# Optimization experiments

Hardware: AMD Instinct MI355X
Metric: run time of the kernel (lower is better)

## Reference

```python
import jax, jax.numpy as jnp
import numpy as np

B, C, T = 8, 256, 8192
CALC, H = 256, 4
D = CALC // H  # head dim = 64
EPS = 1e-5


def setup_inputs() -> dict:
    key = jax.random.key(0)
    ks = jax.random.split(key, 5)
    return {
        "x": jax.random.normal(ks[0], (B, C, T), dtype=jnp.float32),
        "W_prenet": jax.random.normal(ks[1], (3 * CALC, C), dtype=jnp.float32) * 0.05,
        "W_proj": jax.random.normal(ks[2], (C, CALC), dtype=jnp.float32) * 0.05,
        "b_proj": jax.random.normal(ks[3], (C,), dtype=jnp.float32) * 0.05,
        "scale": jax.random.normal(ks[4], (1,), dtype=jnp.float32),
        "gamma": jnp.ones((C,), dtype=jnp.float32),
        "beta": jnp.zeros((C,), dtype=jnp.float32),
    }


def reference(x, W_prenet, W_proj, b_proj, scale, gamma, beta):
    residual = x
    # 1x1 conv prenet: [B, 3*CALC, T]
    h = jnp.einsum('oc,bct->bot', W_prenet, x)
    # split heads: channels grouped as H blocks of 3*D, then chunk into q/k/v of D each
    h = h.reshape(B, H, 3 * D, T)
    q = h[:, :, :D, :]            # [B,H,D,T]
    k = h[:, :, D:2 * D, :]
    v = h[:, :, 2 * D:, :]
    # softmax over time on keys (with the module's +1e-5 shift)
    k = jax.nn.softmax(k + EPS, axis=3)
    # keys @ values^T : [B,H,Dk,Dv]
    kv = jnp.einsum('bhdt,bhet->bhde', k, v)
    # kv^T @ queries  : [B,H,Dv,T]
    ctx = jnp.einsum('bhde,bhdt->bhet', kv, q)
    ctx = ctx.reshape(B, CALC, T)
    # 1x1 conv projection + bias
    out = jnp.einsum('oc,bct->bot', W_proj, ctx) + b_proj[None, :, None]
    out = scale * out  # learnable scalar gate
    # dropout is identity in eval mode
    out = out + residual
    # LayerNorm over channel axis with per-channel affine
    mean = jnp.mean(out, axis=1, keepdims=True)
    var = jnp.var(out, axis=1, keepdims=True)
    out = (out - mean) * jax.lax.rsqrt(var + EPS)
    out = out * gamma[None, :, None] + beta[None, :, None]
    return out
```

## Files before the change

kernel.cpp:

```cpp
#include <hip/hip_runtime.h>
#include <hip/hip_bf16.h>
#include <math.h>

#define BB 8
#define CC 256
#define TT 8192
#define EPSF 1e-5f

typedef short v8s __attribute__((ext_vector_type(8)));
typedef float v4f __attribute__((ext_vector_type(4)));

#define MFMA(a, b, c) __builtin_amdgcn_mfma_f32_16x16x32_bf16((a), (b), (c), 0, 0, 0)


#define OFF_WKV 0
#define OFF_WPJ 65536
#define OFF_UPART 98304
#define OFF_ZPART 4292608
#define OFF_KV 4358144
#define OFF_PT 4489216
#define OFF_MBF 4751360

__device__ __forceinline__ unsigned short f2bf(float f) {
  __hip_bfloat16 h = __float2bfloat16(f);
  return __builtin_bit_cast(unsigned short, h);
}
__device__ __forceinline__ float bf2f(unsigned short u) {
  return __bfloat162float(__builtin_bit_cast(__hip_bfloat16, u));
}

__global__ void k0_pack(const float* __restrict__ Wpre,
                        const float* __restrict__ Wproj,
                        float* __restrict__ ws) {
  const int r = blockIdx.x;
  const int c = threadIdx.x;
  if (r < 512) {
    const int h = r >> 7, type = (r >> 6) & 1, d = r & 63;
    const int src = h * 192 + 64 + type * 64 + d;
    ((unsigned short*)(ws + OFF_WKV))[r * 256 + c] = f2bf(Wpre[(size_t)src * 256 + c]);
  } else {
    const int rr = r - 512;
    ((unsigned short*)(ws + OFF_WPJ))[rr * 256 + c] = f2bf(Wproj[(size_t)rr * 256 + c]);
  }
}

__global__ __launch_bounds__(512, 2) void k1_kv(const float* __restrict__ x,
                                                float* __restrict__ ws) {
  __shared__ unsigned short lds[20480];

  const int tid = threadIdx.x;
  const int w = tid >> 6, lane = tid & 63, q = lane >> 4, cl = lane & 15;
  const int h = w >> 1, type = w & 1;
  const int bi = blockIdx.x;
  const int b = bi >> 5, chunk = bi & 31;
  const int t0 = chunk * 256;
  const float* xb = x + (size_t)b * (CC * TT);
  const unsigned short* wkv =
      (const unsigned short*)(ws + OFF_WKV) + (size_t)((h * 2 + type) * 64) * 256;
  unsigned short* ekb = &lds[h * 5120];
  unsigned short* vbb = &lds[h * 5120 + 2560];

  v4f Uacc[2][4];
#pragma unroll
  for (int i = 0; i < 2; ++i)
#pragma unroll
    for (int j = 0; j < 4; ++j) Uacc[i][j] = (v4f){0.f, 0.f, 0.f, 0.f};
  float zacc[4][4];
#pragma unroll
  for (int i = 0; i < 4; ++i)
#pragma unroll
    for (int j = 0; j < 4; ++j) zacc[i][j] = 0.f;

  for (int sub = 0; sub < 4; ++sub) {
    const int ts = t0 + sub * 64;
    {
      const int c = tid & 255, th = tid >> 8;
      const float* xp = xb + (size_t)c * TT + ts + th * 32;
#pragma unroll
      for (int j = 0; j < 8; ++j) {
        const float4 v4 = reinterpret_cast<const float4*>(xp)[j];
        const int tb = th * 32 + j * 4;
        lds[(tb + 0) * 264 + c] = f2bf(v4.x);
        lds[(tb + 1) * 264 + c] = f2bf(v4.y);
        lds[(tb + 2) * 264 + c] = f2bf(v4.z);
        lds[(tb + 3) * 264 + c] = f2bf(v4.w);
      }
    }
    __syncthreads();

    v4f acc[4][4];
#pragma unroll
    for (int i = 0; i < 4; ++i)
#pragma unroll
      for (int j = 0; j < 4; ++j) acc[i][j] = (v4f){0.f, 0.f, 0.f, 0.f};
#pragma unroll
    for (int ks = 0; ks < 8; ++ks) {
      v8s af[4], bfu[4];
#pragma unroll
      for (int rt = 0; rt < 4; ++rt)
        af[rt] = *(const v8s*)(wkv + (size_t)(rt * 16 + cl) * 256 + ks * 32 + q * 8);
#pragma unroll
      for (int ct = 0; ct < 4; ++ct)
        bfu[ct] = *(const v8s*)&lds[(ct * 16 + cl) * 264 + ks * 32 + q * 8];
#pragma unroll
      for (int rt = 0; rt < 4; ++rt)
#pragma unroll
        for (int ct = 0; ct < 4; ++ct)
          acc[rt][ct] = MFMA(af[rt], bfu[ct], acc[rt][ct]);
    }
    __syncthreads();

#pragma unroll
    for (int hp = 0; hp < 2; ++hp) {
      if (type == 0) {
#pragma unroll
        for (int rt = 0; rt < 4; ++rt)
#pragma unroll
          for (int cc = 0; cc < 2; ++cc) {
            const int ct = hp * 2 + cc;
#pragma unroll
            for (int reg = 0; reg < 4; ++reg) {
              const float e = __expf(acc[rt][ct][reg]);
              zacc[rt][reg] += e;
              ekb[(rt * 16 + q * 4 + reg) * 40 + cc * 16 + cl] = f2bf(e);
            }
          }
      } else {
#pragma unroll
        for (int rt = 0; rt < 4; ++rt)
#pragma unroll
          for (int cc = 0; cc < 2; ++cc) {
            const int ct = hp * 2 + cc;
#pragma unroll
            for (int reg = 0; reg < 4; ++reg)
              vbb[(rt * 16 + q * 4 + reg) * 40 + cc * 16 + cl] =
                  f2bf(acc[rt][ct][reg]);
          }
      }
      __syncthreads();
      {
        const int du0 = type * 32;
        v8s afu[2], bfu[4];
#pragma unroll
        for (int ur = 0; ur < 2; ++ur)
          afu[ur] = *(const v8s*)&ekb[(du0 + ur * 16 + cl) * 40 + q * 8];
#pragma unroll
        for (int uc = 0; uc < 4; ++uc)
          bfu[uc] = *(const v8s*)&vbb[(uc * 16 + cl) * 40 + q * 8];
#pragma unroll
        for (int ur = 0; ur < 2; ++ur)
#pragma unroll
          for (int uc = 0; uc < 4; ++uc)
            Uacc[ur][uc] = MFMA(afu[ur], bfu[uc], Uacc[ur][uc]);
      }
      __syncthreads();
    }
  }

  if (type == 0) {
#pragma unroll
    for (int m = 1; m < 16; m <<= 1)
#pragma unroll
      for (int rt = 0; rt < 4; ++rt)
#pragma unroll
        for (int reg = 0; reg < 4; ++reg)
          zacc[rt][reg] += __shfl_xor(zacc[rt][reg], m, 64);
    if (cl == 0) {
      for (int rt = 0; rt < 4; ++rt)
        for (int reg = 0; reg < 4; ++reg)
          ws[OFF_ZPART + (size_t)bi * 256 + h * 64 + rt * 16 + q * 4 + reg] =
              zacc[rt][reg];
    }
  }
  float* Up = ws + OFF_UPART + (size_t)bi * 16384 + h * 4096;
#pragma unroll
  for (int ur = 0; ur < 2; ++ur)
#pragma unroll
    for (int uc = 0; uc < 4; ++uc)
#pragma unroll
      for (int reg = 0; reg < 4; ++reg)
        Up[(type * 32 + ur * 16 + q * 4 + reg) * 64 + uc * 16 + cl] =
            Uacc[ur][uc][reg];
}

__global__ void k2_reduce_kv(float* __restrict__ ws) {
  const int bi = blockIdx.x;
  const int bh = bi >> 4, j = bi & 15;
  const int b = bh >> 2, h = bh & 3;
  const int tid = threadIdx.x;

  __shared__ float zinv[64];
  if (tid < 64) {
    float z = 0.f;
    for (int cb = 0; cb < 32; ++cb)
      z += ws[OFF_ZPART + (size_t)(b * 32 + cb) * 256 + h * 64 + tid];
    zinv[tid] = 1.0f / z;
  }
  __syncthreads();

  const int idx = j * 256 + tid;
  const int d = idx >> 6;
  float s = 0.f;
  for (int cb = 0; cb < 32; ++cb)
    s += ws[OFF_UPART + (size_t)(b * 32 + cb) * 16384 + h * 4096 + idx];
  ws[OFF_KV + (size_t)(b * 4 + h) * 4096 + idx] = s * zinv[d];
}

__global__ void k3a_P(const float* __restrict__ Wpre, float* __restrict__ ws) {
  const int bi = blockIdx.x;
  const int b = bi >> 8, he = bi & 255;
  const int h = he >> 6, e = he & 63;
  const int c = threadIdx.x;
  const float* kvp = ws + OFF_KV + (size_t)(b * 4 + h) * 4096;
  float acc = 0.f;
#pragma unroll 8
  for (int d = 0; d < 64; ++d)
    acc += kvp[d * 64 + e] * Wpre[(size_t)(h * 192 + d) * 256 + c];
  ((unsigned short*)(ws + OFF_PT))[(size_t)b * 65536 + (size_t)c * 256 + he] =
      f2bf(acc);
}

__global__ __launch_bounds__(256, 2) void k3b_M(const float* __restrict__ scale,
                                                float* __restrict__ ws) {
  const int bi = blockIdx.x, b = bi >> 2, cg = bi & 3;
  const int tid = threadIdx.x, w = tid >> 6, lane = tid & 63, q = lane >> 4,
            cl = lane & 15;
  const unsigned short* wpj = (const unsigned short*)(ws + OFF_WPJ);
  const unsigned short* pt =
      (const unsigned short*)(ws + OFF_PT) + (size_t)b * 65536;
  v4f acc[4][4];
#pragma unroll
  for (int i = 0; i < 4; ++i)
#pragma unroll
    for (int j = 0; j < 4; ++j) acc[i][j] = (v4f){0.f, 0.f, 0.f, 0.f};
#pragma unroll
  for (int ks = 0; ks < 8; ++ks) {
    v8s af[4], bfu[4];
#pragma unroll
    for (int rt = 0; rt < 4; ++rt)
      af[rt] = *(const v8s*)(wpj + (size_t)(w * 64 + rt * 16 + cl) * 256 +
                             ks * 32 + q * 8);
#pragma unroll
    for (int ct = 0; ct < 4; ++ct)
      bfu[ct] = *(const v8s*)(pt + (size_t)(cg * 64 + ct * 16 + cl) * 256 +
                              ks * 32 + q * 8);
#pragma unroll
    for (int rt = 0; rt < 4; ++rt)
#pragma unroll
      for (int ct = 0; ct < 4; ++ct)
        acc[rt][ct] = MFMA(af[rt], bfu[ct], acc[rt][ct]);
  }
  const float s = scale[0];
  unsigned short* mbf = (unsigned short*)(ws + OFF_MBF);
#pragma unroll
  for (int rt = 0; rt < 4; ++rt)
#pragma unroll
    for (int ct = 0; ct < 4; ++ct)
#pragma unroll
      for (int reg = 0; reg < 4; ++reg) {
        const int o = w * 64 + rt * 16 + q * 4 + reg;
        const int c = cg * 64 + ct * 16 + cl;
        mbf[((size_t)b * 256 + o) * 256 + c] = f2bf(s * acc[rt][ct][reg]);
      }
}

__global__ __launch_bounds__(256, 2) void k4_proj_ln(
    const float* __restrict__ x, const float* __restrict__ bproj,
    const float* __restrict__ scale, const float* __restrict__ gamma,
    const float* __restrict__ beta, const float* __restrict__ ws,
    float* __restrict__ out) {
  __shared__ unsigned short xs[64 * 264];
  __shared__ float red1[256], red2[256], muA[64], rsA[64];
  const int bi = blockIdx.x, b = bi >> 7, tc = bi & 127;
  const int tg0 = tc * 64;
  const int tid = threadIdx.x, w = tid >> 6, lane = tid & 63, q = lane >> 4,
            cl = lane & 15;
  const float* xb = x + (size_t)b * (CC * TT);

  {
    const int c = tid;
    const float* xp = xb + (size_t)c * TT + tg0;
#pragma unroll
    for (int j = 0; j < 16; ++j) {
      const float4 v4 = reinterpret_cast<const float4*>(xp)[j];
      const int tb = j * 4;
      xs[(tb + 0) * 264 + c] = f2bf(v4.x);
      xs[(tb + 1) * 264 + c] = f2bf(v4.y);
      xs[(tb + 2) * 264 + c] = f2bf(v4.z);
      xs[(tb + 3) * 264 + c] = f2bf(v4.w);
    }
  }
  __syncthreads();

  const unsigned short* mbf =
      (const unsigned short*)(ws + OFF_MBF) + (size_t)b * 65536;
  v4f acc[4][4];
#pragma unroll
  for (int i = 0; i < 4; ++i)
#pragma unroll
    for (int j = 0; j < 4; ++j) acc[i][j] = (v4f){0.f, 0.f, 0.f, 0.f};
#pragma unroll
  for (int ks = 0; ks < 8; ++ks) {
    v8s af[4], bfu[4];
#pragma unroll
    for (int rt = 0; rt < 4; ++rt)
      af[rt] = *(const v8s*)(mbf + (size_t)(w * 64 + rt * 16 + cl) * 256 +
                             ks * 32 + q * 8);
#pragma unroll
    for (int ct = 0; ct < 4; ++ct)
      bfu[ct] = *(const v8s*)&xs[(ct * 16 + cl) * 264 + ks * 32 + q * 8];
#pragma unroll
    for (int rt = 0; rt < 4; ++rt)
#pragma unroll
      for (int ct = 0; ct < 4; ++ct)
        acc[rt][ct] = MFMA(af[rt], bfu[ct], acc[rt][ct]);
  }

  const float s = scale[0];
#pragma unroll
  for (int rt = 0; rt < 4; ++rt)
#pragma unroll
    for (int reg = 0; reg < 4; ++reg) {
      const int o = w * 64 + rt * 16 + q * 4 + reg;
      const float sb = s * bproj[o];
#pragma unroll
      for (int ct = 0; ct < 4; ++ct) {
        const int tl = ct * 16 + cl;
        acc[rt][ct][reg] += sb + bf2f(xs[tl * 264 + o]);
      }
    }

#pragma unroll
  for (int ct = 0; ct < 4; ++ct) {
    float s1 = 0.f, s2 = 0.f;
#pragma unroll
    for (int rt = 0; rt < 4; ++rt)
#pragma unroll
      for (int reg = 0; reg < 4; ++reg) {
        const float v = acc[rt][ct][reg];
        s1 += v;
        s2 += v * v;
      }
    s1 += __shfl_xor(s1, 16, 64);
    s1 += __shfl_xor(s1, 32, 64);
    s2 += __shfl_xor(s2, 16, 64);
    s2 += __shfl_xor(s2, 32, 64);
    if (q == 0) {
      red1[w * 64 + ct * 16 + cl] = s1;
      red2[w * 64 + ct * 16 + cl] = s2;
    }
  }
  __syncthreads();
  if (tid < 64) {
    const float s1 = red1[tid] + red1[64 + tid] + red1[128 + tid] + red1[192 + tid];
    const float s2 = red2[tid] + red2[64 + tid] + red2[128 + tid] + red2[192 + tid];
    const float mu = s1 * (1.f / 256.f);
    const float var = s2 * (1.f / 256.f) - mu * mu;
    muA[tid] = mu;
    rsA[tid] = rsqrtf(var + EPSF);
  }
  __syncthreads();

  float* ob = out + (size_t)b * (CC * TT) + tg0;
#pragma unroll
  for (int rt = 0; rt < 4; ++rt)
#pragma unroll
    for (int reg = 0; reg < 4; ++reg) {
      const int o = w * 64 + rt * 16 + q * 4 + reg;
      const float g = gamma[o], bt = beta[o];
#pragma unroll
      for (int ct = 0; ct < 4; ++ct) {
        const int tl = ct * 16 + cl;
        ob[(size_t)o * TT + tl] = (acc[rt][ct][reg] - muA[tl]) * rsA[tl] * g + bt;
      }
    }
}

extern "C" void kernel_launch(void* const* d_in, const int* in_sizes, int n_in,
                              void* d_out, int out_size, void* d_ws,
                              size_t ws_size, hipStream_t stream) {
  (void)in_sizes; (void)n_in; (void)out_size; (void)ws_size;
  const float* x = (const float*)d_in[0];
  const float* Wpre = (const float*)d_in[1];
  const float* Wproj = (const float*)d_in[2];
  const float* bproj = (const float*)d_in[3];
  const float* scale = (const float*)d_in[4];
  const float* gamma = (const float*)d_in[5];
  const float* beta = (const float*)d_in[6];
  float* out = (float*)d_out;
  float* ws = (float*)d_ws;

  hipLaunchKernelGGL(k0_pack, dim3(768), dim3(256), 0, stream, Wpre, Wproj, ws);
  hipLaunchKernelGGL(k1_kv, dim3(256), dim3(512), 0, stream, x, ws);
  hipLaunchKernelGGL(k2_reduce_kv, dim3(512), dim3(256), 0, stream, ws);
  hipLaunchKernelGGL(k3a_P, dim3(BB * 256), dim3(256), 0, stream, Wpre, ws);
  hipLaunchKernelGGL(k3b_M, dim3(32), dim3(256), 0, stream, scale, ws);
  hipLaunchKernelGGL(k4_proj_ln, dim3(BB * 128), dim3(256), 0, stream, x, bproj,
                     scale, gamma, beta, ws, out);
}
```

Before: 225.0 us.

## Pre-transpose x to bf16 [T,C] and stream tiles into LDS via global_load_lds

Adds a transpose kernel that converts x once into a bf16 time-major buffer. k1 and k4 then fill their LDS tiles with direct global-to-LDS 16-byte copies in a new padded layout, replacing the per-element fp32 load, convert and scattered LDS store. k1 now uses smaller time chunks across twice as many blocks, and it stores its partial U sums in bf16, halving that reduction traffic in k2. The cost is one extra full pass over x (read fp32, write bf16), higher occupancy targets that may spill registers, and some precision loss from summing partials stored in bf16.

```diff
diff --git a/kernel.cpp b/kernel.cpp
--- a/kernel.cpp
+++ b/kernel.cpp
@@ -13,13 +13,14 @@
 #define MFMA(a, b, c) __builtin_amdgcn_mfma_f32_16x16x32_bf16((a), (b), (c), 0, 0, 0)
 
 
-#define OFF_WKV 0
-#define OFF_WPJ 65536
-#define OFF_UPART 98304
-#define OFF_ZPART 4292608
-#define OFF_KV 4358144
-#define OFF_PT 4489216
-#define OFF_MBF 4751360
+#define OFF_XT 0
+#define OFF_WKV 8388608
+#define OFF_WPJ 8454144
+#define OFF_ZPART 8486912
+#define OFF_KV 8617984
+#define OFF_UPART 8749056
+#define OFF_PT 8749056
+#define OFF_MBF 9011200
 
 __device__ __forceinline__ unsigned short f2bf(float f) {
   __hip_bfloat16 h = __float2bfloat16(f);
@@ -27,6 +28,47 @@
 }
 __device__ __forceinline__ float bf2f(unsigned short u) {
   return __bfloat162float(__builtin_bit_cast(__hip_bfloat16, u));
+}
+
+__device__ __forceinline__ void ldscpy16(unsigned short* lds_base,
+                                         const unsigned short* g_lane) {
+  __builtin_amdgcn_global_load_lds(
+      (const __attribute__((address_space(1))) unsigned int*)(const void*)g_lane,
+      (__attribute__((address_space(3))) unsigned int*)(void*)lds_base, 16, 0, 0);
+}
+
+#define XS_ADDR(t, c) ((((t) >> 1) * 520) + (((t)&1) * 256) + (c))
+
+__global__ __launch_bounds__(256) void kT_transpose(const float* __restrict__ x,
+                                                    float* __restrict__ ws) {
+  __shared__ float lsx[64 * 65];
+  const int bi = blockIdx.x;
+  const int b = bi >> 9;
+  const int cseg = (bi >> 7) & 3;
+  const int tseg = bi & 127;
+  const int c0 = cseg * 64, t0 = tseg * 64;
+  const int tid = threadIdx.x;
+  {
+    const int cl = tid >> 2, q4 = tid & 3;
+    const float* xp = x + (size_t)b * CC * TT + (size_t)(c0 + cl) * TT + t0 + q4 * 16;
+#pragma unroll
+    for (int j = 0; j < 4; ++j) {
+      const float4 v = reinterpret_cast<const float4*>(xp)[j];
+      float* d = &lsx[cl * 65 + q4 * 16 + j * 4];
+      d[0] = v.x; d[1] = v.y; d[2] = v.z; d[3] = v.w;
+    }
+  }
+  __syncthreads();
+  {
+    const int tl = tid >> 2, cs = tid & 3;
+    unsigned short ub[16];
+#pragma unroll
+    for (int j = 0; j < 16; ++j) ub[j] = f2bf(lsx[(cs * 16 + j) * 65 + tl]);
+    unsigned short* xt = (unsigned short*)(ws + OFF_XT) +
+                         ((size_t)b * TT + t0 + tl) * 256 + c0 + cs * 16;
+    reinterpret_cast<int4*>(xt)[0] = *reinterpret_cast<int4*>(&ub[0]);
+    reinterpret_cast<int4*>(xt)[1] = *reinterpret_cast<int4*>(&ub[8]);
+  }
 }
 
 __global__ void k0_pack(const float* __restrict__ Wpre,
@@ -44,17 +86,17 @@
   }
 }
 
-__global__ __launch_bounds__(512, 2) void k1_kv(const float* __restrict__ x,
-                                                float* __restrict__ ws) {
+__global__ __launch_bounds__(512, 4) void k1_kv(float* __restrict__ ws) {
   __shared__ unsigned short lds[20480];
 
   const int tid = threadIdx.x;
   const int w = tid >> 6, lane = tid & 63, q = lane >> 4, cl = lane & 15;
   const int h = w >> 1, type = w & 1;
   const int bi = blockIdx.x;
-  const int b = bi >> 5, chunk = bi & 31;
-  const int t0 = chunk * 256;
-  const float* xb = x + (size_t)b * (CC * TT);
+  const int b = bi >> 6, chunk = bi & 63;
+  const int t0 = chunk * 128;
+  const unsigned short* xT =
+      (const unsigned short*)(ws + OFF_XT) + (size_t)b * TT * 256;
   const unsigned short* wkv =
       (const unsigned short*)(ws + OFF_WKV) + (size_t)((h * 2 + type) * 64) * 256;
   unsigned short* ekb = &lds[h * 5120];
@@ -71,19 +113,13 @@
 #pragma unroll
     for (int j = 0; j < 4; ++j) zacc[i][j] = 0.f;
 
-  for (int sub = 0; sub < 4; ++sub) {
-    const int ts = t0 + sub * 64;
+  for (int sub = 0; sub < 2; ++sub) {
     {
-      const int c = tid & 255, th = tid >> 8;
-      const float* xp = xb + (size_t)c * TT + ts + th * 32;
-#pragma unroll
-      for (int j = 0; j < 8; ++j) {
-        const float4 v4 = reinterpret_cast<const float4*>(xp)[j];
-        const int tb = th * 32 + j * 4;
-        lds[(tb + 0) * 264 + c] = f2bf(v4.x);
-        lds[(tb + 1) * 264 + c] = f2bf(v4.y);
-        lds[(tb + 2) * 264 + c] = f2bf(v4.z);
-        lds[(tb + 3) * 264 + c] = f2bf(v4.w);
+      const unsigned short* xsrc = xT + (size_t)(t0 + sub * 64) * 256 + lane * 8;
+#pragma unroll
+      for (int i = 0; i < 4; ++i) {
+        const int pair = w * 4 + i;
+        ldscpy16(&lds[pair * 520], xsrc + pair * 512);
       }
     }
     __syncthreads();
@@ -100,8 +136,10 @@
       for (int rt = 0; rt < 4; ++rt)
         af[rt] = *(const v8s*)(wkv + (size_t)(rt * 16 + cl) * 256 + ks * 32 + q * 8);
 #pragma unroll
-      for (int ct = 0; ct < 4; ++ct)
-        bfu[ct] = *(const v8s*)&lds[(ct * 16 + cl) * 264 + ks * 32 + q * 8];
+      for (int ct = 0; ct < 4; ++ct) {
+        const int t = ct * 16 + cl;
+        bfu[ct] = *(const v8s*)&lds[XS_ADDR(t, ks * 32 + q * 8)];
+      }
 #pragma unroll
       for (int rt = 0; rt < 4; ++rt)
 #pragma unroll
@@ -172,7 +210,8 @@
               zacc[rt][reg];
     }
   }
-  float* Up = ws + OFF_UPART + (size_t)bi * 16384 + h * 4096;
+  unsigned short* Up =
+      (unsigned short*)(ws + OFF_UPART) + (size_t)bi * 16384 + h * 4096;
 #pragma unroll
   for (int ur = 0; ur < 2; ++ur)
 #pragma unroll
@@ -180,7 +219,7 @@
 #pragma unroll
       for (int reg = 0; reg < 4; ++reg)
         Up[(type * 32 + ur * 16 + q * 4 + reg) * 64 + uc * 16 + cl] =
-            Uacc[ur][uc][reg];
+            f2bf(Uacc[ur][uc][reg]);
 }
 
 __global__ void k2_reduce_kv(float* __restrict__ ws) {
@@ -192,17 +231,18 @@
   __shared__ float zinv[64];
   if (tid < 64) {
     float z = 0.f;
-    for (int cb = 0; cb < 32; ++cb)
-      z += ws[OFF_ZPART + (size_t)(b * 32 + cb) * 256 + h * 64 + tid];
+    for (int cb = 0; cb < 64; ++cb)
+      z += ws[OFF_ZPART + (size_t)(b * 64 + cb) * 256 + h * 64 + tid];
     zinv[tid] = 1.0f / z;
   }
   __syncthreads();
 
   const int idx = j * 256 + tid;
   const int d = idx >> 6;
+  const unsigned short* up = (const unsigned short*)(ws + OFF_UPART);
   float s = 0.f;
-  for (int cb = 0; cb < 32; ++cb)
-    s += ws[OFF_UPART + (size_t)(b * 32 + cb) * 16384 + h * 4096 + idx];
+  for (int cb = 0; cb < 64; ++cb)
+    s += bf2f(up[(size_t)(b * 64 + cb) * 16384 + h * 4096 + idx]);
   ws[OFF_KV + (size_t)(b * 4 + h) * 4096 + idx] = s * zinv[d];
 }
 
@@ -264,30 +304,24 @@
       }
 }
 
-__global__ __launch_bounds__(256, 2) void k4_proj_ln(
-    const float* __restrict__ x, const float* __restrict__ bproj,
-    const float* __restrict__ scale, const float* __restrict__ gamma,
-    const float* __restrict__ beta, const float* __restrict__ ws,
-    float* __restrict__ out) {
-  __shared__ unsigned short xs[64 * 264];
+__global__ __launch_bounds__(256, 4) void k4_proj_ln(
+    const float* __restrict__ bproj, const float* __restrict__ scale,
+    const float* __restrict__ gamma, const float* __restrict__ beta,
+    const float* __restrict__ ws, float* __restrict__ out) {
+  __shared__ unsigned short xs[16640];
   __shared__ float red1[256], red2[256], muA[64], rsA[64];
   const int bi = blockIdx.x, b = bi >> 7, tc = bi & 127;
   const int tg0 = tc * 64;
   const int tid = threadIdx.x, w = tid >> 6, lane = tid & 63, q = lane >> 4,
             cl = lane & 15;
-  const float* xb = x + (size_t)b * (CC * TT);
 
   {
-    const int c = tid;
-    const float* xp = xb + (size_t)c * TT + tg0;
-#pragma unroll
-    for (int j = 0; j < 16; ++j) {
-      const float4 v4 = reinterpret_cast<const float4*>(xp)[j];
-      const int tb = j * 4;
-      xs[(tb + 0) * 264 + c] = f2bf(v4.x);
-      xs[(tb + 1) * 264 + c] = f2bf(v4.y);
-      xs[(tb + 2) * 264 + c] = f2bf(v4.z);
-      xs[(tb + 3) * 264 + c] = f2bf(v4.w);
+    const unsigned short* xsrc = (const unsigned short*)(ws + OFF_XT) +
+                                 ((size_t)b * TT + tg0) * 256 + lane * 8;
+#pragma unroll
+    for (int i = 0; i < 8; ++i) {
+      const int pair = w * 8 + i;
+      ldscpy16(&xs[pair * 520], xsrc + pair * 512);
     }
   }
   __syncthreads();
@@ -307,8 +341,10 @@
       af[rt] = *(const v8s*)(mbf + (size_t)(w * 64 + rt * 16 + cl) * 256 +
                              ks * 32 + q * 8);
 #pragma unroll
-    for (int ct = 0; ct < 4; ++ct)
-      bfu[ct] = *(const v8s*)&xs[(ct * 16 + cl) * 264 + ks * 32 + q * 8];
+    for (int ct = 0; ct < 4; ++ct) {
+      const int t = ct * 16 + cl;
+      bfu[ct] = *(const v8s*)&xs[XS_ADDR(t, ks * 32 + q * 8)];
+    }
 #pragma unroll
     for (int rt = 0; rt < 4; ++rt)
 #pragma unroll
@@ -326,7 +362,7 @@
 #pragma unroll
       for (int ct = 0; ct < 4; ++ct) {
         const int tl = ct * 16 + cl;
-        acc[rt][ct][reg] += sb + bf2f(xs[tl * 264 + o]);
+        acc[rt][ct][reg] += sb + bf2f(xs[XS_ADDR(tl, o)]);
       }
     }
 
@@ -390,11 +426,12 @@
   float* out = (float*)d_out;
   float* ws = (float*)d_ws;
 
+  hipLaunchKernelGGL(kT_transpose, dim3(4096), dim3(256), 0, stream, x, ws);
   hipLaunchKernelGGL(k0_pack, dim3(768), dim3(256), 0, stream, Wpre, Wproj, ws);
-  hipLaunchKernelGGL(k1_kv, dim3(256), dim3(512), 0, stream, x, ws);
+  hipLaunchKernelGGL(k1_kv, dim3(512), dim3(512), 0, stream, ws);
   hipLaunchKernelGGL(k2_reduce_kv, dim3(512), dim3(256), 0, stream, ws);
   hipLaunchKernelGGL(k3a_P, dim3(BB * 256), dim3(256), 0, stream, Wpre, ws);
   hipLaunchKernelGGL(k3b_M, dim3(32), dim3(256), 0, stream, scale, ws);
-  hipLaunchKernelGGL(k4_proj_ln, dim3(BB * 128), dim3(256), 0, stream, x, bproj,
+  hipLaunchKernelGGL(k4_proj_ln, dim3(BB * 128), dim3(256), 0, stream, bproj,
                      scale, gamma, beta, ws, out);
 }
```

New measurement: 278.6 us. 1.24x slower.
